# Optimization experiments

Measured on AMD Instinct MI355X. Metric: run time of the kernel, lower is better.

## Reference

```python
import jax, jax.numpy as jnp
import numpy as np

B, S, H = 1, 2048, 2880
NH, NKV, HD = 64, 8, 64
WIN = 128
ROPE_BASE = 10000.0


def setup_inputs() -> dict:
    key = jax.random.key(0)
    ks = jax.random.split(key, 8)

    def lin(k, fi, fo):
        return (jax.random.normal(k, (fi, fo), jnp.float32) / np.sqrt(fi)).astype(jnp.float32)

    hidden_states = jax.random.normal(ks[0], (B, S, H), jnp.float32)
    Wq = lin(ks[1], H, NH * HD)
    Wk = lin(ks[2], H, NKV * HD)
    Wv = lin(ks[3], H, NKV * HD)
    Wo = lin(ks[4], NH * HD, H)
    bq = jnp.zeros((NH * HD,), jnp.float32)
    bk = jnp.zeros((NKV * HD,), jnp.float32)
    bv = jnp.zeros((NKV * HD,), jnp.float32)
    bo = jnp.zeros((H,), jnp.float32)
    sinks = jax.random.normal(ks[5], (NH,), jnp.float32) * 0.5

    # RoPE tables, shape [B, S, HD] (rotate_half convention: halves duplicated)
    pos = jnp.arange(S, dtype=jnp.float32)
    inv_freq = 1.0 / (ROPE_BASE ** (jnp.arange(0, HD, 2, dtype=jnp.float32) / HD))
    freqs = pos[:, None] * inv_freq[None, :]          # [S, HD/2]
    emb = jnp.concatenate([freqs, freqs], axis=-1)    # [S, HD]
    cos = jnp.broadcast_to(jnp.cos(emb)[None], (B, S, HD))
    sin = jnp.broadcast_to(jnp.sin(emb)[None], (B, S, HD))

    return dict(hidden_states=hidden_states, cos=cos, sin=sin,
                Wq=Wq, bq=bq, Wk=Wk, bk=bk, Wv=Wv, bv=bv, Wo=Wo, bo=bo,
                sinks=sinks, window=WIN)


def _rotate_half(x):
    x1, x2 = jnp.split(x, 2, axis=-1)
    return jnp.concatenate([-x2, x1], axis=-1)


def reference(hidden_states, cos, sin, Wq, bq, Wk, bk, Wv, bv, Wo, bo, sinks, window):
    b, s, _ = hidden_states.shape
    nh = sinks.shape[0]
    hd = Wq.shape[1] // nh
    nkv = Wk.shape[1] // hd
    scale = hd ** -0.5

    q = (hidden_states @ Wq + bq).reshape(b, s, nh, hd)
    k = (hidden_states @ Wk + bk).reshape(b, s, nkv, hd)
    v = (hidden_states @ Wv + bv).reshape(b, s, nkv, hd)

    c = cos[:, :, None, :]  # [b, s, 1, hd]
    sn = sin[:, :, None, :]
    q = q * c + _rotate_half(q) * sn
    k = k * c + _rotate_half(k) * sn

    # GQA: expand kv heads to query heads
    g = nh // nkv
    k_rep = jnp.repeat(k, g, axis=2)  # [b, s, nh, hd]
    v_rep = jnp.repeat(v, g, axis=2)

    scores = jnp.einsum('bqhd,bkhd->bhqk', q, k_rep) * scale  # [b, nh, s, s]

    # causal sliding-window mask
    qi = jnp.arange(s)[:, None]
    ki = jnp.arange(s)[None, :]
    allowed = (qi >= ki) & (qi - ki < window)
    neg = jnp.finfo(scores.dtype).min
    scores = jnp.where(allowed[None, None], scores, neg)

    # virtual sink column at kv index s: score replaced by learned per-head bias
    sink_col = jnp.broadcast_to(sinks[None, :, None, None], (b, nh, s, 1))
    scores = jnp.concatenate([scores, sink_col], axis=-1)  # [b, nh, s, s+1]

    probs = jax.nn.softmax(scores, axis=-1)
    # sink value vector is zeros, so only real columns contribute
    out = jnp.einsum('bhqk,bkhd->bqhd', probs[..., :s], v_rep)
    out = out.reshape(b, s, nh * hd) @ Wo + bo
    return out
```

## Files before the change

kernel.cpp:

```cpp
#include <hip/hip_runtime.h>
#include <stdint.h>
#include <stddef.h>

typedef unsigned short u16;
typedef unsigned int u32;
typedef float f32x4 __attribute__((ext_vector_type(4)));
typedef __bf16 bf16x8 __attribute__((ext_vector_type(8)));
typedef uint32_t u32x4 __attribute__((ext_vector_type(4)));
typedef uint32_t u32x2 __attribute__((ext_vector_type(2)));

#define DEVINL static __device__ __forceinline__
#define VMW(n) asm volatile("s_waitcnt vmcnt(" #n ")" ::: "memory")
#define LGK0() asm volatile("s_waitcnt lgkmcnt(0)" ::: "memory")
#define SB0() __builtin_amdgcn_sched_barrier(0)

DEVINL u16 f2bf(float f) {
  union { float f; u32 u; } x; x.f = f;
  u32 r = (x.u + 0x7fffu + ((x.u >> 16) & 1u)) >> 16;
  return (u16)r;
}
DEVINL float bflo(u32 x) { union { u32 u; float f; } t; t.u = x << 16; return t.f; }
DEVINL float bfhi(u32 x) { union { u32 u; float f; } t; t.u = x & 0xffff0000u; return t.f; }

DEVINL void gl_lds16(const u16* g, u16* l) {
  __builtin_amdgcn_global_load_lds(
      (const __attribute__((address_space(1))) u32*)(const void*)g,
      (__attribute__((address_space(3))) u32*)(void*)l, 16, 0, 0);
}

DEVINL f32x4 mfma16(bf16x8 a, bf16x8 b, f32x4 c) {
  return __builtin_amdgcn_mfma_f32_16x16x32_bf16(a, b, c, 0, 0, 0);
}

__global__ void k_cvt(const float* __restrict__ src, u16* __restrict__ dst, int n4) {
  int i = blockIdx.x * 256 + threadIdx.x;
  if (i >= n4) return;
  f32x4 v = ((const f32x4*)src)[i];
  u32x2 o;
  o[0] = (u32)f2bf(v[0]) | ((u32)f2bf(v[1]) << 16);
  o[1] = (u32)f2bf(v[2]) | ((u32)f2bf(v[3]) << 16);
  ((u32x2*)dst)[i] = o;
}

__global__ void k_tcvt(const float* __restrict__ src, u16* __restrict__ dst, int R, int C) {
  __shared__ float tile[32][33];
  int tx = threadIdx.x, ty = threadIdx.y;
  int c0 = blockIdx.x * 32, r0 = blockIdx.y * 32;
#pragma unroll
  for (int j = ty; j < 32; j += 8)
    tile[j][tx] = src[(size_t)(r0 + j) * C + (c0 + tx)];
  __syncthreads();
#pragma unroll
  for (int j = ty; j < 32; j += 8)
    dst[(size_t)(c0 + j) * R + (r0 + tx)] = f2bf(tile[tx][j]);
}

__global__ __launch_bounds__(256, 2) void k_gemmq(
    const u16* __restrict__ A, const u16* __restrict__ Bgl, u16* __restrict__ Cout,
    const float* __restrict__ pb0, const float* __restrict__ pb1, const float* __restrict__ pb2)
{
  constexpr int K = 2880, NT = 45, LDC = 5120;
  __shared__ u16 Asm[2][128 * 64];
  __shared__ u16 Bsm[2][160 * 64];

  const int bid = blockIdx.x;
  const int swz = (bid & 7) * 64 + (bid >> 3);
  const int bx = swz >> 4, by = swz & 15;
  const int m0 = by * 128, n0 = bx * 160;

  const int tid = threadIdx.x;
  const int w = tid >> 6, lane = tid & 63;
  const int l15 = lane & 15, lg = lane >> 4;
  const int wr = w >> 1, wc = w & 1;

  const u16* Ag = A + (size_t)m0 * K;
  const u16* Bg = Bgl + (size_t)n0 * K;

  auto ld1 = [&](const u16* s, u16* d, int slot) {
    int row = slot >> 3, c = slot & 7;
    gl_lds16(s + (size_t)row * K + ((c ^ (row & 7)) << 3), d + row * 64 + c * 8);
  };
  auto stApart = [&](int tg, int part) {
    u16* d = Asm[tg & 1];
    const u16* s = Ag + tg * 64;
    ld1(s, d, part * 256 + tid);
    ld1(s, d, part * 256 + 512 + tid);
  };
  auto stBa = [&](int tg) {
    u16* d = Bsm[tg & 1];
    const u16* s = Bg + tg * 64;
    ld1(s, d, tid);
    ld1(s, d, 640 + tid);
  };
  auto stBb = [&](int tg) {
    u16* d = Bsm[tg & 1];
    const u16* s = Bg + tg * 64;
    ld1(s, d, 256 + tid);
    ld1(s, d, (tid < 128) ? (512 + tid) : (768 + tid));
    ld1(s, d, 1024 + tid);
  };

  const int ra = wr * 64 + l15;
  const int rb = wc * 80 + l15;
  const int x0 = (lg ^ (l15 & 7)) << 3;
  const int x1 = x0 ^ 32;

  f32x4 acc[4][5] = {};
  bf16x8 af[2][2], bfr[5][2];

  stBa(0); stBb(0); stApart(0, 0); stApart(0, 1);
  VMW(2);
  __builtin_amdgcn_s_barrier();
  SB0();

  for (int t = 0; t < NT; ++t) {
    const u16* Ab = Asm[t & 1];
    const u16* Bb_ = Bsm[t & 1];
    const bool st = (t + 1 < NT);
#pragma unroll
    for (int m = 0; m < 2; ++m) {
      af[m][0] = *(const bf16x8*)&Ab[(ra + m * 16) * 64 + x0];
      af[m][1] = *(const bf16x8*)&Ab[(ra + m * 16) * 64 + x1];
    }
#pragma unroll
    for (int n = 0; n < 2; ++n) {
      bfr[n][0] = *(const bf16x8*)&Bb_[(rb + n * 16) * 64 + x0];
      bfr[n][1] = *(const bf16x8*)&Bb_[(rb + n * 16) * 64 + x1];
    }
    if (st) stBa(t + 1);
    LGK0(); SB0();
    __builtin_amdgcn_s_setprio(1);
#pragma unroll
    for (int kk = 0; kk < 2; ++kk)
#pragma unroll
      for (int m = 0; m < 2; ++m)
#pragma unroll
        for (int n = 0; n < 2; ++n)
          acc[m][n] = mfma16(af[m][kk], bfr[n][kk], acc[m][n]);
    __builtin_amdgcn_s_setprio(0);
#pragma unroll
    for (int n = 2; n < 5; ++n) {
      bfr[n][0] = *(const bf16x8*)&Bb_[(rb + n * 16) * 64 + x0];
      bfr[n][1] = *(const bf16x8*)&Bb_[(rb + n * 16) * 64 + x1];
    }
    if (st) stBb(t + 1);
    LGK0(); SB0();
    __builtin_amdgcn_s_setprio(1);
#pragma unroll
    for (int kk = 0; kk < 2; ++kk)
#pragma unroll
      for (int m = 0; m < 2; ++m)
#pragma unroll
        for (int n = 2; n < 5; ++n)
          acc[m][n] = mfma16(af[m][kk], bfr[n][kk], acc[m][n]);
    __builtin_amdgcn_s_setprio(0);
    if (st) { VMW(5); } else { VMW(0); }
    __builtin_amdgcn_s_barrier();
    SB0();
#pragma unroll
    for (int m = 0; m < 2; ++m) {
      af[m][0] = *(const bf16x8*)&Ab[(ra + 32 + m * 16) * 64 + x0];
      af[m][1] = *(const bf16x8*)&Ab[(ra + 32 + m * 16) * 64 + x1];
    }
    if (st) stApart(t + 1, 0);
    LGK0(); SB0();
    __builtin_amdgcn_s_setprio(1);
#pragma unroll
    for (int kk = 0; kk < 2; ++kk)
#pragma unroll
      for (int m = 0; m < 2; ++m)
#pragma unroll
        for (int n = 0; n < 2; ++n)
          acc[2 + m][n] = mfma16(af[m][kk], bfr[n][kk], acc[2 + m][n]);
    __builtin_amdgcn_s_setprio(0);
    if (st) stApart(t + 1, 1);
    __builtin_amdgcn_s_setprio(1);
#pragma unroll
    for (int kk = 0; kk < 2; ++kk)
#pragma unroll
      for (int m = 0; m < 2; ++m)
#pragma unroll
        for (int n = 2; n < 5; ++n)
          acc[2 + m][n] = mfma16(af[m][kk], bfr[n][kk], acc[2 + m][n]);
    __builtin_amdgcn_s_setprio(0);
    VMW(2);
    __builtin_amdgcn_s_barrier();
    SB0();
  }

#pragma unroll
  for (int m2 = 0; m2 < 4; ++m2)
#pragma unroll
    for (int n = 0; n < 5; ++n) {
      int col = n0 + wc * 80 + n * 16 + l15;
      float bias = (col < 4096) ? pb0[col] : (col < 4608) ? pb1[col - 4096] : pb2[col - 4608];
#pragma unroll
      for (int q = 0; q < 4; ++q) {
        int row = m0 + wr * 64 + m2 * 16 + lg * 4 + q;
        Cout[(size_t)row * LDC + col] = f2bf(acc[m2][n][q] + bias);
      }
    }
}

__global__ __launch_bounds__(256, 2) void k_gemmo(
    const u16* __restrict__ A, const u16* __restrict__ Bgl, float* __restrict__ Cout,
    const float* __restrict__ pb0)
{
  constexpr int K = 4096, NT = 64, LDC = 2880;
  __shared__ u16 Asm[2][128 * 64];
  __shared__ u16 Bsm[2][96 * 64];

  const int bid = blockIdx.x;
  const int swz = (bid & 7) * 60 + (bid >> 3);
  const int bx = swz / 16, by = swz & 15;
  const int m0 = by * 128, n0 = bx * 96;

  const int tid = threadIdx.x;
  const int w = tid >> 6, lane = tid & 63;
  const int l15 = lane & 15, lg = lane >> 4;
  const int wr = w >> 1, wc = w & 1;

  const u16* Ag = A + (size_t)m0 * K;
  const u16* Bg = Bgl + (size_t)n0 * K;

  auto ld1 = [&](const u16* s, u16* d, int slot) {
    int row = slot >> 3, c = slot & 7;
    gl_lds16(s + (size_t)row * K + ((c ^ (row & 7)) << 3), d + row * 64 + c * 8);
  };
  auto stApart = [&](int tg, int part) {
    u16* d = Asm[tg & 1];
    const u16* s = Ag + tg * 64;
    ld1(s, d, part * 256 + tid);
    ld1(s, d, part * 256 + 512 + tid);
  };
  auto stB = [&](int tg) {
    u16* d = Bsm[tg & 1];
    const u16* s = Bg + tg * 64;
    ld1(s, d, tid);
    ld1(s, d, 256 + tid);
    ld1(s, d, 512 + tid);
  };

  const int ra = wr * 64 + l15;
  const int rb = wc * 48 + l15;
  const int x0 = (lg ^ (l15 & 7)) << 3;
  const int x1 = x0 ^ 32;

  f32x4 acc[4][3] = {};
  bf16x8 af[2][2], bfr[3][2];

  stB(0); stApart(0, 0); stApart(0, 1);
  VMW(2);
  __builtin_amdgcn_s_barrier();
  SB0();

  for (int t = 0; t < NT; ++t) {
    const u16* Ab = Asm[t & 1];
    const u16* Bb_ = Bsm[t & 1];
    const bool st = (t + 1 < NT);
#pragma unroll
    for (int m = 0; m < 2; ++m) {
      af[m][0] = *(const bf16x8*)&Ab[(ra + m * 16) * 64 + x0];
      af[m][1] = *(const bf16x8*)&Ab[(ra + m * 16) * 64 + x1];
    }
#pragma unroll
    for (int n = 0; n < 3; ++n) {
      bfr[n][0] = *(const bf16x8*)&Bb_[(rb + n * 16) * 64 + x0];
      bfr[n][1] = *(const bf16x8*)&Bb_[(rb + n * 16) * 64 + x1];
    }
    if (st) { stB(t + 1); stApart(t + 1, 0); }
    LGK0(); SB0();
    __builtin_amdgcn_s_setprio(1);
#pragma unroll
    for (int kk = 0; kk < 2; ++kk)
#pragma unroll
      for (int m = 0; m < 2; ++m)
#pragma unroll
        for (int n = 0; n < 3; ++n)
          acc[m][n] = mfma16(af[m][kk], bfr[n][kk], acc[m][n]);
    __builtin_amdgcn_s_setprio(0);
    if (st) { VMW(5); } else { VMW(0); }
    __builtin_amdgcn_s_barrier();
    SB0();
#pragma unroll
    for (int m = 0; m < 2; ++m) {
      af[m][0] = *(const bf16x8*)&Ab[(ra + 32 + m * 16) * 64 + x0];
      af[m][1] = *(const bf16x8*)&Ab[(ra + 32 + m * 16) * 64 + x1];
    }
    if (st) stApart(t + 1, 1);
    LGK0(); SB0();
    __builtin_amdgcn_s_setprio(1);
#pragma unroll
    for (int kk = 0; kk < 2; ++kk)
#pragma unroll
      for (int m = 0; m < 2; ++m)
#pragma unroll
        for (int n = 0; n < 3; ++n)
          acc[2 + m][n] = mfma16(af[m][kk], bfr[n][kk], acc[2 + m][n]);
    __builtin_amdgcn_s_setprio(0);
    VMW(2);
    __builtin_amdgcn_s_barrier();
    SB0();
  }

#pragma unroll
  for (int m2 = 0; m2 < 4; ++m2)
#pragma unroll
    for (int n = 0; n < 3; ++n) {
      int col = n0 + wc * 48 + n * 16 + l15;
      float bias = pb0[col];
#pragma unroll
      for (int q = 0; q < 4; ++q) {
        int row = m0 + wr * 64 + m2 * 16 + lg * 4 + q;
        Cout[(size_t)row * LDC + col] = acc[m2][n][q] + bias;
      }
    }
}

__global__ void k_rope(u16* __restrict__ qkv, const float* __restrict__ cosb,
                       const float* __restrict__ sinb) {
  int idx = blockIdx.x * 256 + threadIdx.x;
  if (idx >= 2048 * 72 * 4) return;
  int oct = idx & 3;
  int h = (idx >> 2) % 72;
  int s = idx / 288;
  u16* p1 = qkv + (size_t)s * 5120 + h * 64 + oct * 8;
  u16* p2 = p1 + 32;
  const float* pc = cosb + (size_t)s * 64 + oct * 8;
  const float* ps = sinb + (size_t)s * 64 + oct * 8;
  u32x4 a = *(const u32x4*)p1;
  u32x4 b = *(const u32x4*)p2;
  f32x4 c0 = *(const f32x4*)pc, c1 = *(const f32x4*)(pc + 4);
  f32x4 s0 = *(const f32x4*)ps, s1 = *(const f32x4*)(ps + 4);
  float C[8] = {c0[0], c0[1], c0[2], c0[3], c1[0], c1[1], c1[2], c1[3]};
  float Sn[8] = {s0[0], s0[1], s0[2], s0[3], s1[0], s1[1], s1[2], s1[3]};
  u32x4 ra, rb;
#pragma unroll
  for (int i = 0; i < 4; ++i) {
    float x1l = bflo(a[i]), x1h = bfhi(a[i]);
    float x2l = bflo(b[i]), x2h = bfhi(b[i]);
    float o1l = x1l * C[2 * i] - x2l * Sn[2 * i];
    float o1h = x1h * C[2 * i + 1] - x2h * Sn[2 * i + 1];
    float o2l = x2l * C[2 * i] + x1l * Sn[2 * i];
    float o2h = x2h * C[2 * i + 1] + x1h * Sn[2 * i + 1];
    ra[i] = (u32)f2bf(o1l) | ((u32)f2bf(o1h) << 16);
    rb[i] = (u32)f2bf(o2l) | ((u32)f2bf(o2h) << 16);
  }
  *(u32x4*)p1 = ra;
  *(u32x4*)p2 = rb;
}

__global__ __launch_bounds__(512, 1) void k_attn(
    const u16* __restrict__ qkv, const float* __restrict__ sinks, u16* __restrict__ aout)
{
  __shared__ u16 Kl[160 * 64];
  __shared__ u16 Vt[64 * 168];
  __shared__ u16 Pl[8][2][16][40];

  const int qt = blockIdx.x * 32;
  const int kv = blockIdx.y;
  const int tid = threadIdx.x;
  const int w = tid >> 6, lane = tid & 63;
  const int l15 = lane & 15, lg = lane >> 4;

  for (int idx = tid; idx < 160 * 8; idx += 512) {
    int row = idx >> 3, ch = idx & 7;
    int key = qt - 128 + row;
    u32x4 val = {0, 0, 0, 0};
    if (key >= 0) val = *(const u32x4*)(qkv + (size_t)key * 5120 + 4096 + kv * 64 + ch * 8);
    *(u32x4*)((char*)Kl + row * 128 + ((ch * 16) ^ ((row & 7) << 4))) = val;
  }
  for (int idx = tid; idx < 160 * 8; idx += 512) {
    int row = idx >> 3, ch = idx & 7;
    int key = qt - 128 + row;
    u32x4 val = {0, 0, 0, 0};
    if (key >= 0) val = *(const u32x4*)(qkv + (size_t)key * 5120 + 4608 + kv * 64 + ch * 8);
    const u16* pv16 = (const u16*)&val;
#pragma unroll
    for (int j = 0; j < 8; ++j) Vt[(ch * 8 + j) * 168 + row] = pv16[j];
  }
  __syncthreads();

  const int h = kv * 8 + w;
  const float sink = sinks[h];

  bf16x8 qf[2][2];
#pragma unroll
  for (int rt = 0; rt < 2; ++rt)
#pragma unroll
    for (int ks = 0; ks < 2; ++ks)
      qf[rt][ks] = *(const bf16x8*)(qkv + (size_t)(qt + rt * 16 + l15) * 5120 + h * 64 + ks * 32 + lg * 8);

  f32x4 S[2][5][2];
#pragma unroll
  for (int kb = 0; kb < 5; ++kb)
#pragma unroll
    for (int hh = 0; hh < 2; ++hh) {
      int krow = kb * 32 + hh * 16 + l15;
      int sw = (krow & 7) << 4;
      bf16x8 kf0 = *(const bf16x8*)((const char*)Kl + krow * 128 + ((lg * 16) ^ sw));
      bf16x8 kf1 = *(const bf16x8*)((const char*)Kl + krow * 128 + ((64 + lg * 16) ^ sw));
#pragma unroll
      for (int rt = 0; rt < 2; ++rt) {
        f32x4 a = {0.f, 0.f, 0.f, 0.f};
        a = mfma16(qf[rt][0], kf0, a);
        a = mfma16(qf[rt][1], kf1, a);
        S[rt][kb][hh] = a;
      }
    }

  float inv_s[2][4];
#pragma unroll
  for (int rt = 0; rt < 2; ++rt)
#pragma unroll
    for (int r = 0; r < 4; ++r) {
      int q_abs = qt + rt * 16 + lg * 4 + r;
      float m = -1e30f;
#pragma unroll
      for (int kb = 0; kb < 5; ++kb)
#pragma unroll
        for (int hh = 0; hh < 2; ++hh) {
          int k_abs = qt - 128 + kb * 32 + hh * 16 + l15;
          float v = S[rt][kb][hh][r] * 0.125f;
          bool ok = (k_abs >= 0) && (k_abs <= q_abs) && (q_abs - k_abs < 128);
          v = ok ? v : -1e30f;
          S[rt][kb][hh][r] = v;
          m = fmaxf(m, v);
        }
      m = fmaxf(m, __shfl_xor(m, 1, 64));
      m = fmaxf(m, __shfl_xor(m, 2, 64));
      m = fmaxf(m, __shfl_xor(m, 4, 64));
      m = fmaxf(m, __shfl_xor(m, 8, 64));
      m = fmaxf(m, sink);
      float sum = 0.f;
#pragma unroll
      for (int kb = 0; kb < 5; ++kb)
#pragma unroll
        for (int hh = 0; hh < 2; ++hh) {
          float p = __expf(S[rt][kb][hh][r] - m);
          S[rt][kb][hh][r] = p;
          sum += p;
        }
      sum += __shfl_xor(sum, 1, 64);
      sum += __shfl_xor(sum, 2, 64);
      sum += __shfl_xor(sum, 4, 64);
      sum += __shfl_xor(sum, 8, 64);
      inv_s[rt][r] = 1.0f / (sum + __expf(sink - m));
    }

  f32x4 pv[2][4] = {};
#pragma unroll
  for (int kb = 0; kb < 5; ++kb) {
    asm volatile("s_waitcnt lgkmcnt(0)" ::: "memory");
#pragma unroll
    for (int rt = 0; rt < 2; ++rt)
#pragma unroll
      for (int hh = 0; hh < 2; ++hh)
#pragma unroll
        for (int r = 0; r < 4; ++r)
          Pl[w][rt][lg * 4 + r][hh * 16 + l15] = f2bf(S[rt][kb][hh][r] * inv_s[rt][r]);
    asm volatile("s_waitcnt lgkmcnt(0)" ::: "memory");
    __builtin_amdgcn_sched_barrier(0);
    bf16x8 a0 = *(const bf16x8*)&Pl[w][0][l15][lg * 8];
    bf16x8 a1 = *(const bf16x8*)&Pl[w][1][l15][lg * 8];
#pragma unroll
    for (int nt = 0; nt < 4; ++nt) {
      bf16x8 vf = *(const bf16x8*)&Vt[(nt * 16 + l15) * 168 + kb * 32 + lg * 8];
      pv[0][nt] = mfma16(a0, vf, pv[0][nt]);
      pv[1][nt] = mfma16(a1, vf, pv[1][nt]);
    }
  }

#pragma unroll
  for (int rt = 0; rt < 2; ++rt)
#pragma unroll
    for (int nt = 0; nt < 4; ++nt)
#pragma unroll
      for (int r = 0; r < 4; ++r)
        aout[(size_t)(qt + rt * 16 + lg * 4 + r) * 4096 + h * 64 + nt * 16 + l15] =
            f2bf(pv[rt][nt][r]);
}

extern "C" void kernel_launch(void* const* d_in, const int* in_sizes, int n_in,
                              void* d_out, int out_size, void* d_ws, size_t ws_size,
                              hipStream_t stream) {
  const float* hs    = (const float*)d_in[0];
  const float* cosb  = (const float*)d_in[1];
  const float* sinb  = (const float*)d_in[2];
  const float* Wq    = (const float*)d_in[3];
  const float* bq    = (const float*)d_in[4];
  const float* Wk    = (const float*)d_in[5];
  const float* bk    = (const float*)d_in[6];
  const float* Wv    = (const float*)d_in[7];
  const float* bv    = (const float*)d_in[8];
  const float* Wo    = (const float*)d_in[9];
  const float* bo    = (const float*)d_in[10];
  const float* sinks = (const float*)d_in[11];

  char* ws = (char*)d_ws;
  u16* hsb   = (u16*)ws;  ws += (size_t)2048 * 2880 * 2;
  u16* WqkvT = (u16*)ws;  ws += (size_t)5120 * 2880 * 2;
  u16* WoT   = (u16*)ws;  ws += (size_t)2880 * 4096 * 2;
  u16* QKV   = (u16*)ws;  ws += (size_t)2048 * 5120 * 2;
  u16* AOut  = (u16*)ws;  ws += (size_t)2048 * 4096 * 2;

  dim3 tblk(32, 8);
  k_cvt<<<5760, 256, 0, stream>>>(hs, hsb, 1474560);
  k_tcvt<<<dim3(4096 / 32, 2880 / 32), tblk, 0, stream>>>(Wq, WqkvT, 2880, 4096);
  k_tcvt<<<dim3(512 / 32, 2880 / 32), tblk, 0, stream>>>(Wk, WqkvT + (size_t)4096 * 2880, 2880, 512);
  k_tcvt<<<dim3(512 / 32, 2880 / 32), tblk, 0, stream>>>(Wv, WqkvT + (size_t)4608 * 2880, 2880, 512);
  k_tcvt<<<dim3(2880 / 32, 4096 / 32), tblk, 0, stream>>>(Wo, WoT, 4096, 2880);

  k_gemmq<<<512, 256, 0, stream>>>(hsb, WqkvT, QKV, bq, bk, bv);

  k_rope<<<2304, 256, 0, stream>>>(QKV, cosb, sinb);

  k_attn<<<dim3(64, 8), 512, 0, stream>>>(QKV, sinks, AOut);

  k_gemmo<<<480, 256, 0, stream>>>(AOut, WoT, (float*)d_out, bo);
}
```

Measured before the change: 196.5 us.

## Vectorize weight transpose-convert with 64x64 tiles and double attention query tile

Replaces the 32x32 transpose-convert kernel with a 64x64 tiled version that uses 16-byte float4 loads and 16-byte packed bf16 stores, to cut memory transactions when converting the weights. The attention kernel now handles 64 queries per block in two 32-query passes over one staged 192-row K/V window. This reuses the overlapping sliding-window keys and values and halves the redundant K/V staging. The trade-off is half as many attention blocks, which could reduce occupancy across the CUs.

```diff
diff --git a/kernel.cpp b/kernel.cpp
--- a/kernel.cpp
+++ b/kernel.cpp
@@ -42,17 +42,39 @@
   ((u32x2*)dst)[i] = o;
 }
 
-__global__ void k_tcvt(const float* __restrict__ src, u16* __restrict__ dst, int R, int C) {
-  __shared__ float tile[32][33];
-  int tx = threadIdx.x, ty = threadIdx.y;
-  int c0 = blockIdx.x * 32, r0 = blockIdx.y * 32;
-#pragma unroll
-  for (int j = ty; j < 32; j += 8)
-    tile[j][tx] = src[(size_t)(r0 + j) * C + (c0 + tx)];
+__global__ __launch_bounds__(256) void k_tcvt2(const float* __restrict__ src,
+                                               u16* __restrict__ dst, int R, int C) {
+  __shared__ float t[64][65];
+  const int tid = threadIdx.x;
+  const int r0 = blockIdx.y * 64, c0 = blockIdx.x * 64;
+  {
+    const int rr = tid >> 2, cg = (tid & 3) * 16;
+    const float* s = src + (size_t)(r0 + rr) * C + c0 + cg;
+#pragma unroll
+    for (int i = 0; i < 4; ++i) {
+      f32x4 v = *(const f32x4*)(s + 4 * i);
+      t[rr][cg + 4 * i + 0] = v[0];
+      t[rr][cg + 4 * i + 1] = v[1];
+      t[rr][cg + 4 * i + 2] = v[2];
+      t[rr][cg + 4 * i + 3] = v[3];
+    }
+  }
   __syncthreads();
-#pragma unroll
-  for (int j = ty; j < 32; j += 8)
-    dst[(size_t)(c0 + j) * R + (r0 + tx)] = f2bf(tile[tx][j]);
+  {
+    const int rg = tid & 7, cb = tid >> 3;
+#pragma unroll
+    for (int it = 0; it < 2; ++it) {
+      const int c = cb + it * 32;
+      float v[8];
+#pragma unroll
+      for (int i = 0; i < 8; ++i) v[i] = t[rg * 8 + i][c];
+      u32x4 o;
+#pragma unroll
+      for (int j = 0; j < 4; ++j)
+        o[j] = (u32)f2bf(v[2 * j]) | ((u32)f2bf(v[2 * j + 1]) << 16);
+      *(u32x4*)(dst + (size_t)(c0 + c) * R + r0 + rg * 8) = o;
+    }
+  }
 }
 
 __global__ __launch_bounds__(256, 2) void k_gemmq(
@@ -353,132 +375,135 @@
 __global__ __launch_bounds__(512, 1) void k_attn(
     const u16* __restrict__ qkv, const float* __restrict__ sinks, u16* __restrict__ aout)
 {
-  __shared__ u16 Kl[160 * 64];
-  __shared__ u16 Vt[64 * 168];
+  __shared__ u16 Kl[192 * 64];
+  __shared__ u16 Vt[64 * 200];
   __shared__ u16 Pl[8][2][16][40];
 
-  const int qt = blockIdx.x * 32;
+  const int qt = blockIdx.x * 64;
   const int kv = blockIdx.y;
   const int tid = threadIdx.x;
   const int w = tid >> 6, lane = tid & 63;
   const int l15 = lane & 15, lg = lane >> 4;
 
-  for (int idx = tid; idx < 160 * 8; idx += 512) {
+  for (int idx = tid; idx < 192 * 8; idx += 512) {
     int row = idx >> 3, ch = idx & 7;
     int key = qt - 128 + row;
     u32x4 val = {0, 0, 0, 0};
     if (key >= 0) val = *(const u32x4*)(qkv + (size_t)key * 5120 + 4096 + kv * 64 + ch * 8);
     *(u32x4*)((char*)Kl + row * 128 + ((ch * 16) ^ ((row & 7) << 4))) = val;
   }
-  for (int idx = tid; idx < 160 * 8; idx += 512) {
+  for (int idx = tid; idx < 192 * 8; idx += 512) {
     int row = idx >> 3, ch = idx & 7;
     int key = qt - 128 + row;
     u32x4 val = {0, 0, 0, 0};
     if (key >= 0) val = *(const u32x4*)(qkv + (size_t)key * 5120 + 4608 + kv * 64 + ch * 8);
     const u16* pv16 = (const u16*)&val;
 #pragma unroll
-    for (int j = 0; j < 8; ++j) Vt[(ch * 8 + j) * 168 + row] = pv16[j];
+    for (int j = 0; j < 8; ++j) Vt[(ch * 8 + j) * 200 + row] = pv16[j];
   }
   __syncthreads();
 
   const int h = kv * 8 + w;
   const float sink = sinks[h];
 
-  bf16x8 qf[2][2];
-#pragma unroll
-  for (int rt = 0; rt < 2; ++rt)
-#pragma unroll
-    for (int ks = 0; ks < 2; ++ks)
-      qf[rt][ks] = *(const bf16x8*)(qkv + (size_t)(qt + rt * 16 + l15) * 5120 + h * 64 + ks * 32 + lg * 8);
-
-  f32x4 S[2][5][2];
-#pragma unroll
-  for (int kb = 0; kb < 5; ++kb)
-#pragma unroll
-    for (int hh = 0; hh < 2; ++hh) {
-      int krow = kb * 32 + hh * 16 + l15;
-      int sw = (krow & 7) << 4;
-      bf16x8 kf0 = *(const bf16x8*)((const char*)Kl + krow * 128 + ((lg * 16) ^ sw));
-      bf16x8 kf1 = *(const bf16x8*)((const char*)Kl + krow * 128 + ((64 + lg * 16) ^ sw));
-#pragma unroll
-      for (int rt = 0; rt < 2; ++rt) {
-        f32x4 a = {0.f, 0.f, 0.f, 0.f};
-        a = mfma16(qf[rt][0], kf0, a);
-        a = mfma16(qf[rt][1], kf1, a);
-        S[rt][kb][hh] = a;
+  for (int qs = 0; qs < 2; ++qs) {
+    const int qb = qt + qs * 32;
+    bf16x8 qf[2][2];
+#pragma unroll
+    for (int rt = 0; rt < 2; ++rt)
+#pragma unroll
+      for (int ks = 0; ks < 2; ++ks)
+        qf[rt][ks] = *(const bf16x8*)(qkv + (size_t)(qb + rt * 16 + l15) * 5120 + h * 64 + ks * 32 + lg * 8);
+
+    f32x4 S[2][5][2];
+#pragma unroll
+    for (int kb = 0; kb < 5; ++kb)
+#pragma unroll
+      for (int hh = 0; hh < 2; ++hh) {
+        int krow = qs * 32 + kb * 32 + hh * 16 + l15;
+        int sw = (krow & 7) << 4;
+        bf16x8 kf0 = *(const bf16x8*)((const char*)Kl + krow * 128 + ((lg * 16) ^ sw));
+        bf16x8 kf1 = *(const bf16x8*)((const char*)Kl + krow * 128 + ((64 + lg * 16) ^ sw));
+#pragma unroll
+        for (int rt = 0; rt < 2; ++rt) {
+          f32x4 a = {0.f, 0.f, 0.f, 0.f};
+          a = mfma16(qf[rt][0], kf0, a);
+          a = mfma16(qf[rt][1], kf1, a);
+          S[rt][kb][hh] = a;
+        }
       }
-    }
-
-  float inv_s[2][4];
-#pragma unroll
-  for (int rt = 0; rt < 2; ++rt)
-#pragma unroll
-    for (int r = 0; r < 4; ++r) {
-      int q_abs = qt + rt * 16 + lg * 4 + r;
-      float m = -1e30f;
-#pragma unroll
-      for (int kb = 0; kb < 5; ++kb)
-#pragma unroll
-        for (int hh = 0; hh < 2; ++hh) {
-          int k_abs = qt - 128 + kb * 32 + hh * 16 + l15;
-          float v = S[rt][kb][hh][r] * 0.125f;
-          bool ok = (k_abs >= 0) && (k_abs <= q_abs) && (q_abs - k_abs < 128);
-          v = ok ? v : -1e30f;
-          S[rt][kb][hh][r] = v;
-          m = fmaxf(m, v);
-        }
-      m = fmaxf(m, __shfl_xor(m, 1, 64));
-      m = fmaxf(m, __shfl_xor(m, 2, 64));
-      m = fmaxf(m, __shfl_xor(m, 4, 64));
-      m = fmaxf(m, __shfl_xor(m, 8, 64));
-      m = fmaxf(m, sink);
-      float sum = 0.f;
-#pragma unroll
-      for (int kb = 0; kb < 5; ++kb)
-#pragma unroll
-        for (int hh = 0; hh < 2; ++hh) {
-          float p = __expf(S[rt][kb][hh][r] - m);
-          S[rt][kb][hh][r] = p;
-          sum += p;
-        }
-      sum += __shfl_xor(sum, 1, 64);
-      sum += __shfl_xor(sum, 2, 64);
-      sum += __shfl_xor(sum, 4, 64);
-      sum += __shfl_xor(sum, 8, 64);
-      inv_s[rt][r] = 1.0f / (sum + __expf(sink - m));
-    }
-
-  f32x4 pv[2][4] = {};
-#pragma unroll
-  for (int kb = 0; kb < 5; ++kb) {
-    asm volatile("s_waitcnt lgkmcnt(0)" ::: "memory");
+
+    float inv_s[2][4];
 #pragma unroll
     for (int rt = 0; rt < 2; ++rt)
 #pragma unroll
-      for (int hh = 0; hh < 2; ++hh)
+      for (int r = 0; r < 4; ++r) {
+        int q_abs = qb + rt * 16 + lg * 4 + r;
+        float m = -1e30f;
+#pragma unroll
+        for (int kb = 0; kb < 5; ++kb)
+#pragma unroll
+          for (int hh = 0; hh < 2; ++hh) {
+            int k_abs = qb - 128 + kb * 32 + hh * 16 + l15;
+            float v = S[rt][kb][hh][r] * 0.125f;
+            bool ok = (k_abs >= 0) && (k_abs <= q_abs) && (q_abs - k_abs < 128);
+            v = ok ? v : -1e30f;
+            S[rt][kb][hh][r] = v;
+            m = fmaxf(m, v);
+          }
+        m = fmaxf(m, __shfl_xor(m, 1, 64));
+        m = fmaxf(m, __shfl_xor(m, 2, 64));
+        m = fmaxf(m, __shfl_xor(m, 4, 64));
+        m = fmaxf(m, __shfl_xor(m, 8, 64));
+        m = fmaxf(m, sink);
+        float sum = 0.f;
+#pragma unroll
+        for (int kb = 0; kb < 5; ++kb)
+#pragma unroll
+          for (int hh = 0; hh < 2; ++hh) {
+            float p = __expf(S[rt][kb][hh][r] - m);
+            S[rt][kb][hh][r] = p;
+            sum += p;
+          }
+        sum += __shfl_xor(sum, 1, 64);
+        sum += __shfl_xor(sum, 2, 64);
+        sum += __shfl_xor(sum, 4, 64);
+        sum += __shfl_xor(sum, 8, 64);
+        inv_s[rt][r] = 1.0f / (sum + __expf(sink - m));
+      }
+
+    f32x4 pv[2][4] = {};
+#pragma unroll
+    for (int kb = 0; kb < 5; ++kb) {
+      asm volatile("s_waitcnt lgkmcnt(0)" ::: "memory");
+#pragma unroll
+      for (int rt = 0; rt < 2; ++rt)
+#pragma unroll
+        for (int hh = 0; hh < 2; ++hh)
+#pragma unroll
+          for (int r = 0; r < 4; ++r)
+            Pl[w][rt][lg * 4 + r][hh * 16 + l15] = f2bf(S[rt][kb][hh][r] * inv_s[rt][r]);
+      asm volatile("s_waitcnt lgkmcnt(0)" ::: "memory");
+      __builtin_amdgcn_sched_barrier(0);
+      bf16x8 a0 = *(const bf16x8*)&Pl[w][0][l15][lg * 8];
+      bf16x8 a1 = *(const bf16x8*)&Pl[w][1][l15][lg * 8];
+#pragma unroll
+      for (int nt = 0; nt < 4; ++nt) {
+        bf16x8 vf = *(const bf16x8*)&Vt[(nt * 16 + l15) * 200 + qs * 32 + kb * 32 + lg * 8];
+        pv[0][nt] = mfma16(a0, vf, pv[0][nt]);
+        pv[1][nt] = mfma16(a1, vf, pv[1][nt]);
+      }
+    }
+
+#pragma unroll
+    for (int rt = 0; rt < 2; ++rt)
+#pragma unroll
+      for (int nt = 0; nt < 4; ++nt)
 #pragma unroll
         for (int r = 0; r < 4; ++r)
-          Pl[w][rt][lg * 4 + r][hh * 16 + l15] = f2bf(S[rt][kb][hh][r] * inv_s[rt][r]);
-    asm volatile("s_waitcnt lgkmcnt(0)" ::: "memory");
-    __builtin_amdgcn_sched_barrier(0);
-    bf16x8 a0 = *(const bf16x8*)&Pl[w][0][l15][lg * 8];
-    bf16x8 a1 = *(const bf16x8*)&Pl[w][1][l15][lg * 8];
-#pragma unroll
-    for (int nt = 0; nt < 4; ++nt) {
-      bf16x8 vf = *(const bf16x8*)&Vt[(nt * 16 + l15) * 168 + kb * 32 + lg * 8];
-      pv[0][nt] = mfma16(a0, vf, pv[0][nt]);
-      pv[1][nt] = mfma16(a1, vf, pv[1][nt]);
-    }
-  }
-
-#pragma unroll
-  for (int rt = 0; rt < 2; ++rt)
-#pragma unroll
-    for (int nt = 0; nt < 4; ++nt)
-#pragma unroll
-      for (int r = 0; r < 4; ++r)
-        aout[(size_t)(qt + rt * 16 + lg * 4 + r) * 4096 + h * 64 + nt * 16 + l15] =
-            f2bf(pv[rt][nt][r]);
+          aout[(size_t)(qb + rt * 16 + lg * 4 + r) * 4096 + h * 64 + nt * 16 + l15] =
+              f2bf(pv[rt][nt][r]);
+  }
 }
 
 extern "C" void kernel_launch(void* const* d_in, const int* in_sizes, int n_in,
@@ -504,18 +529,17 @@
   u16* QKV   = (u16*)ws;  ws += (size_t)2048 * 5120 * 2;
   u16* AOut  = (u16*)ws;  ws += (size_t)2048 * 4096 * 2;
 
-  dim3 tblk(32, 8);
   k_cvt<<<5760, 256, 0, stream>>>(hs, hsb, 1474560);
-  k_tcvt<<<dim3(4096 / 32, 2880 / 32), tblk, 0, stream>>>(Wq, WqkvT, 2880, 4096);
-  k_tcvt<<<dim3(512 / 32, 2880 / 32), tblk, 0, stream>>>(Wk, WqkvT + (size_t)4096 * 2880, 2880, 512);
-  k_tcvt<<<dim3(512 / 32, 2880 / 32), tblk, 0, stream>>>(Wv, WqkvT + (size_t)4608 * 2880, 2880, 512);
-  k_tcvt<<<dim3(2880 / 32, 4096 / 32), tblk, 0, stream>>>(Wo, WoT, 4096, 2880);
+  k_tcvt2<<<dim3(4096 / 64, 2880 / 64), 256, 0, stream>>>(Wq, WqkvT, 2880, 4096);
+  k_tcvt2<<<dim3(512 / 64, 2880 / 64), 256, 0, stream>>>(Wk, WqkvT + (size_t)4096 * 2880, 2880, 512);
+  k_tcvt2<<<dim3(512 / 64, 2880 / 64), 256, 0, stream>>>(Wv, WqkvT + (size_t)4608 * 2880, 2880, 512);
+  k_tcvt2<<<dim3(2880 / 64, 4096 / 64), 256, 0, stream>>>(Wo, WoT, 4096, 2880);
 
   k_gemmq<<<512, 256, 0, stream>>>(hsb, WqkvT, QKV, bq, bk, bv);
 
   k_rope<<<2304, 256, 0, stream>>>(QKV, cosb, sinb);
 
-  k_attn<<<dim3(64, 8), 512, 0, stream>>>(QKV, sinks, AOut);
+  k_attn<<<dim3(32, 8), 512, 0, stream>>>(QKV, sinks, AOut);
 
   k_gemmo<<<480, 256, 0, stream>>>(AOut, WoT, (float*)d_out, bo);
 }
```

Result: faster. 182.2 us (-7.3%).
